# Kernel tuning notes

Measured on AMD Instinct MI355X. Metric: run time of the kernel, lower is better.

## Reference

```python
import jax, jax.numpy as jnp
import numpy as np

# Conv hyperparams (from init_kwargs)
STRIDE = (1, 1)
PADDING = (1, 1)
DILATION = (1, 1)

AQMIN, AQMAX = 0.0, 15.0   # uint4 activation range
WQMIN, WQMAX = -8.0, 7.0   # int4 weight range


def setup_inputs() -> dict:
    key = jax.random.key(0)
    k1, k2 = jax.random.split(key)
    # Activations in [0, 16) so uint4 quantization is non-trivial
    x = jax.random.uniform(k1, (32, 64, 112, 112), dtype=jnp.float32) * 16.0
    # Weights spread over int4 range
    w = jax.random.normal(k2, (128, 64, 3, 3), dtype=jnp.float32) * 4.0
    return {"x": x, "w": w}


def reference(x, w):
    # Quantize: activations -> uint4 [0,15], weights -> int4 [-8,7]
    q_in = jnp.clip(jnp.round(x), AQMIN, AQMAX)
    q_w = jnp.clip(jnp.round(w), WQMIN, WQMAX)
    # im2col unfold + matmul in the original == standard convolution.
    # Integer-valued fp32 math is exact here (|acc| << 2^24).
    out = jax.lax.conv_general_dilated(
        q_in, q_w,
        window_strides=STRIDE,
        padding=[(PADDING[0], PADDING[0]), (PADDING[1], PADDING[1])],
        rhs_dilation=DILATION,
        dimension_numbers=("NCHW", "OIHW", "NCHW"),
    )
    return out.astype(jnp.float32)  # [32, 128, 112, 112]
```

## Files before the change

kernel.cpp:

```cpp
#include <hip/hip_runtime.h>


#define CIN  64
#define HH   112
#define WW   112
#define HW   (HH * WW)
#define COUT 128
#define HP   114
#define WP   114
#define KTOT 576

#define XQ_BYTES (32 * HP * WP * 64)
#define NWBLK 288
#define NXBLK (32 * 57)
#define NCONV (32 * HH)

#define ROWB (WP * 64)
#define SLAB_BYTES (3 * ROWB)
#define SLAB_U16   (SLAB_BYTES / 16)

typedef __attribute__((ext_vector_type(4))) int int32x4;

__global__ __launch_bounds__(256) void k_prep(const float* __restrict__ x,
                                              const float* __restrict__ w,
                                              char* __restrict__ xq,
                                              char* __restrict__ wq) {
    const int bid = blockIdx.x, tid = threadIdx.x;
    if (bid < NWBLK) {
        int idx = bid * 256 + tid;
        int ks  = idx / 8192;
        int r2  = idx % 8192;
        int ct  = r2 / 1024;
        int r3  = r2 % 1024;
        int ln  = r3 / 16;
        int j   = r3 % 16;
        int o   = ct * 16 + (ln & 15);
        int c   = (ln >> 4) * 16 + j;
        int kh  = ks / 3, kw = ks % 3;
        float q = fminf(fmaxf(rintf(w[((o * CIN + c) * 3 + kh) * 3 + kw]), -8.0f), 7.0f);
        wq[idx] = (char)(int)q;
        return;
    }
    const int rid = bid - NWBLK;
    const int n  = rid / 57;
    const int hp = (rid % 57) * 2 + (tid >> 7);
    const int wp = tid & 127;
    if (wp >= WP) return;
    char* dst = xq + (((size_t)n * HP + hp) * WP + wp) * 64;
    int32x4* d4 = (int32x4*)dst;
    if (hp == 0 || hp == HP - 1 || wp == 0 || wp == WP - 1) {
#pragma unroll
        for (int i = 0; i < 4; ++i) d4[i] = (int32x4)(0);
        return;
    }
    const int h = hp - 1, ww = wp - 1;
    const float* px = x + (((size_t)n * CIN) * HH + h) * WW + ww;
    unsigned int buf[16];
#pragma unroll
    for (int cw = 0; cw < 16; ++cw) {
        unsigned int word = 0;
#pragma unroll
        for (int j = 0; j < 4; ++j) {
            float v = px[(size_t)(cw * 4 + j) * HW];
            float q = fminf(fmaxf(rintf(v), 0.0f), 15.0f);
            word |= ((unsigned int)(int)q) << (8 * j);
        }
        buf[cw] = word;
    }
#pragma unroll
    for (int i = 0; i < 4; ++i) {
        int32x4 v;
        v.x = (int)buf[i * 4 + 0];
        v.y = (int)buf[i * 4 + 1];
        v.z = (int)buf[i * 4 + 2];
        v.w = (int)buf[i * 4 + 3];
        d4[i] = v;
    }
}

__global__ __launch_bounds__(256, 4) void k_conv(const char* __restrict__ xq,
                                                 const char* __restrict__ wq,
                                                 float* __restrict__ out) {
    __shared__ char slab[SLAB_BYTES];

    const int tid = threadIdx.x;
    const int nid = (blockIdx.x & 7) * (NCONV / 8) + (blockIdx.x >> 3);
    const int n   = nid / HH;
    const int h   = nid % HH;

    const char* src = xq + (size_t)n * (HP * ROWB) + (size_t)h * ROWB;
#pragma unroll
    for (int k = 0; k < 6; ++k) {
        const int u = tid + k * 256;
        if (u < SLAB_U16)
            *(int32x4*)(&slab[u * 16]) = *(const int32x4*)(src + u * 16);
    }
    __syncthreads();

    const int wave = tid >> 6;
    const int lane = tid & 63;
    const int l15  = lane & 15;
    const int lk   = lane >> 4;
    const int Q    = wave;

    const char* wbase = wq + (Q * 2) * 1024 + lane * 16;

    int32x4 acc[7][2];
#pragma unroll
    for (int i = 0; i < 7; ++i) {
        acc[i][0] = (int32x4)(0);
        acc[i][1] = (int32x4)(0);
    }

    int32x4 b0[2], b1[2], b2[2];
    b0[0] = *(const int32x4*)(wbase);
    b0[1] = *(const int32x4*)(wbase + 1024);
    b1[0] = *(const int32x4*)(wbase + 8192);
    b1[1] = *(const int32x4*)(wbase + 8192 + 1024);

#pragma unroll
    for (int ks = 0; ks < 9; ++ks) {
        {
            const int ksn = (ks + 2 <= 8) ? ks + 2 : 8;
            b2[0] = *(const int32x4*)(wbase + ksn * 8192);
            b2[1] = *(const int32x4*)(wbase + ksn * 8192 + 1024);
        }
        const int kh = ks / 3, kw = ks % 3;
        const char* arow = &slab[((kh * WP) + l15 + kw) * 64 + lk * 16];
        int32x4 af[7];
#pragma unroll
        for (int wt = 0; wt < 7; ++wt)
            af[wt] = *(const int32x4*)(arow + wt * 1024);
#pragma unroll
        for (int tO = 0; tO < 2; ++tO)
#pragma unroll
            for (int wt = 0; wt < 7; ++wt)
                acc[wt][tO] = __builtin_amdgcn_mfma_i32_16x16x64_i8(af[wt], b0[tO], acc[wt][tO], 0, 0, 0);
        b0[0] = b1[0]; b0[1] = b1[1];
        b1[0] = b2[0]; b1[1] = b2[1];
    }

#pragma unroll
    for (int wt = 0; wt < 7; ++wt) {
#pragma unroll
        for (int tO = 0; tO < 2; ++tO) {
            const int co = Q * 32 + tO * 16 + l15;
            float4 v;
            v.x = (float)acc[wt][tO][0];
            v.y = (float)acc[wt][tO][1];
            v.z = (float)acc[wt][tO][2];
            v.w = (float)acc[wt][tO][3];
            *(float4*)(&out[(((size_t)n * COUT + co) * HH + h) * WW + wt * 16 + lk * 4]) = v;
        }
    }
}

extern "C" void kernel_launch(void* const* d_in, const int* in_sizes, int n_in,
                              void* d_out, int out_size, void* d_ws, size_t ws_size,
                              hipStream_t stream) {
    const float* x = (const float*)d_in[0];
    const float* w = (const float*)d_in[1];
    float* out = (float*)d_out;

    char* xq = (char*)d_ws;
    char* wq = xq + XQ_BYTES;

    hipLaunchKernelGGL(k_prep, dim3(NWBLK + NXBLK), dim3(256), 0, stream, x, w, xq, wq);
    hipLaunchKernelGGL(k_conv, dim3(NCONV), dim3(256), 0, stream, xq, wq, out);
}
```

Before: 92.14 us.

## Preload all conv weights into registers and stream output tiles per width chunk

The conv kernel now loads all nine kernel-position weight fragments into registers before the LDS slab load, so weight global loads overlap with the slab fill. The loop order changes from kernel position outer to width tile outer: each width tile loads its nine activation fragments, runs 18 MFMAs into two accumulators, and stores its output right away. This cuts the live accumulator count from 14 vectors to 2 and interleaves stores with compute. In exchange, weight register use grows and the MFMA dependency chains per accumulator become longer. Launch bounds drop from 4 to 3 blocks per CU.

Result: faster. 87.02 us, median of 2 (-5.6%).

```diff
diff --git a/kernel.cpp b/kernel.cpp
--- a/kernel.cpp
+++ b/kernel.cpp
@@ -78,7 +78,7 @@
     }
 }
 
-__global__ __launch_bounds__(256, 4) void k_conv(const char* __restrict__ xq,
+__global__ __launch_bounds__(256, 3) void k_conv(const char* __restrict__ xq,
                                                  const char* __restrict__ wq,
                                                  float* __restrict__ out) {
     __shared__ char slab[SLAB_BYTES];
@@ -87,6 +87,20 @@
     const int nid = (blockIdx.x & 7) * (NCONV / 8) + (blockIdx.x >> 3);
     const int n   = nid / HH;
     const int h   = nid % HH;
+
+    const int wave = tid >> 6;
+    const int lane = tid & 63;
+    const int l15  = lane & 15;
+    const int lk   = lane >> 4;
+    const int Q    = wave;
+
+    const char* wbase = wq + (Q * 2) * 1024 + lane * 16;
+    int32x4 wreg[9][2];
+#pragma unroll
+    for (int ks = 0; ks < 9; ++ks) {
+        wreg[ks][0] = *(const int32x4*)(wbase + ks * 8192);
+        wreg[ks][1] = *(const int32x4*)(wbase + ks * 8192 + 1024);
+    }
 
     const char* src = xq + (size_t)n * (HP * ROWB) + (size_t)h * ROWB;
 #pragma unroll
@@ -97,61 +111,28 @@
     }
     __syncthreads();
 
-    const int wave = tid >> 6;
-    const int lane = tid & 63;
-    const int l15  = lane & 15;
-    const int lk   = lane >> 4;
-    const int Q    = wave;
-
-    const char* wbase = wq + (Q * 2) * 1024 + lane * 16;
-
-    int32x4 acc[7][2];
-#pragma unroll
-    for (int i = 0; i < 7; ++i) {
-        acc[i][0] = (int32x4)(0);
-        acc[i][1] = (int32x4)(0);
-    }
-
-    int32x4 b0[2], b1[2], b2[2];
-    b0[0] = *(const int32x4*)(wbase);
-    b0[1] = *(const int32x4*)(wbase + 1024);
-    b1[0] = *(const int32x4*)(wbase + 8192);
-    b1[1] = *(const int32x4*)(wbase + 8192 + 1024);
-
-#pragma unroll
-    for (int ks = 0; ks < 9; ++ks) {
-        {
-            const int ksn = (ks + 2 <= 8) ? ks + 2 : 8;
-            b2[0] = *(const int32x4*)(wbase + ksn * 8192);
-            b2[1] = *(const int32x4*)(wbase + ksn * 8192 + 1024);
-        }
-        const int kh = ks / 3, kw = ks % 3;
-        const char* arow = &slab[((kh * WP) + l15 + kw) * 64 + lk * 16];
-        int32x4 af[7];
-#pragma unroll
-        for (int wt = 0; wt < 7; ++wt)
-            af[wt] = *(const int32x4*)(arow + wt * 1024);
-#pragma unroll
-        for (int tO = 0; tO < 2; ++tO)
-#pragma unroll
-            for (int wt = 0; wt < 7; ++wt)
-                acc[wt][tO] = __builtin_amdgcn_mfma_i32_16x16x64_i8(af[wt], b0[tO], acc[wt][tO], 0, 0, 0);
-        b0[0] = b1[0]; b0[1] = b1[1];
-        b1[0] = b2[0]; b1[1] = b2[1];
-    }
+    float* obase = out + (((size_t)n * COUT + Q * 32 + l15) * HH + h) * WW + lk * 4;
 
 #pragma unroll
     for (int wt = 0; wt < 7; ++wt) {
+        int32x4 af[9];
 #pragma unroll
-        for (int tO = 0; tO < 2; ++tO) {
-            const int co = Q * 32 + tO * 16 + l15;
-            float4 v;
-            v.x = (float)acc[wt][tO][0];
-            v.y = (float)acc[wt][tO][1];
-            v.z = (float)acc[wt][tO][2];
-            v.w = (float)acc[wt][tO][3];
-            *(float4*)(&out[(((size_t)n * COUT + co) * HH + h) * WW + wt * 16 + lk * 4]) = v;
+        for (int ks = 0; ks < 9; ++ks) {
+            const int kh = ks / 3, kw = ks % 3;
+            af[ks] = *(const int32x4*)(&slab[((kh * WP) + wt * 16 + l15 + kw) * 64 + lk * 16]);
         }
+        int32x4 a0 = (int32x4)(0);
+        int32x4 a1 = (int32x4)(0);
+#pragma unroll
+        for (int ks = 0; ks < 9; ++ks) {
+            a0 = __builtin_amdgcn_mfma_i32_16x16x64_i8(af[ks], wreg[ks][0], a0, 0, 0, 0);
+            a1 = __builtin_amdgcn_mfma_i32_16x16x64_i8(af[ks], wreg[ks][1], a1, 0, 0, 0);
+        }
+        float4 v0, v1;
+        v0.x = (float)a0[0]; v0.y = (float)a0[1]; v0.z = (float)a0[2]; v0.w = (float)a0[3];
+        v1.x = (float)a1[0]; v1.y = (float)a1[1]; v1.z = (float)a1[2]; v1.w = (float)a1[3];
+        *(float4*)(obase + wt * 16)            = v0;
+        *(float4*)(obase + 16 * HW + wt * 16)  = v1;
     }
 }
 
```

## Fuse activation quantization and conv into persistent kernel with per-image flags

Applied to the files above, without the earlier changes.

Moves activation quantization out of the prep kernel into a persistent main kernel (768 blocks) that first processes quantize items and then conv items. Each conv item spins on a per-image atomic counter until all 57 row-pair blocks of that image are written, so conv work for early images can overlap quantization of later ones. This removes the kernel boundary between the quantize and conv stages. In exchange it adds spin-waiting, acquire/release fences, and a residency assumption: the persistent grid must be co-resident or the spin-waits could deadlock.

New measurement: 334.9 us. +263.4%, slower.

```diff
diff --git a/kernel.cpp b/kernel.cpp
--- a/kernel.cpp
+++ b/kernel.cpp
@@ -11,9 +11,13 @@
 #define KTOT 576
 
 #define XQ_BYTES (32 * HP * WP * 64)
+#define WQ_BYTES (COUT * KTOT)
 #define NWBLK 288
-#define NXBLK (32 * 57)
-#define NCONV (32 * HH)
+
+#define NACT   (32 * 57)
+#define NCONVI (32 * HH)
+#define NITEMS (NACT + NCONVI)
+#define GPERS  768
 
 #define ROWB (WP * 64)
 #define SLAB_BYTES (3 * ROWB)
@@ -21,10 +25,9 @@
 
 typedef __attribute__((ext_vector_type(4))) int int32x4;
 
-__global__ __launch_bounds__(256) void k_prep(const float* __restrict__ x,
-                                              const float* __restrict__ w,
-                                              char* __restrict__ xq,
-                                              char* __restrict__ wq) {
+__global__ __launch_bounds__(256) void k_init(const float* __restrict__ w,
+                                              char* __restrict__ wq,
+                                              int* __restrict__ flags) {
     const int bid = blockIdx.x, tid = threadIdx.x;
     if (bid < NWBLK) {
         int idx = bid * 256 + tid;
@@ -41,116 +44,136 @@
         wq[idx] = (char)(int)q;
         return;
     }
-    const int rid = bid - NWBLK;
-    const int n  = rid / 57;
-    const int hp = (rid % 57) * 2 + (tid >> 7);
-    const int wp = tid & 127;
-    if (wp >= WP) return;
-    char* dst = xq + (((size_t)n * HP + hp) * WP + wp) * 64;
-    int32x4* d4 = (int32x4*)dst;
-    if (hp == 0 || hp == HP - 1 || wp == 0 || wp == WP - 1) {
-#pragma unroll
-        for (int i = 0; i < 4; ++i) d4[i] = (int32x4)(0);
-        return;
-    }
-    const int h = hp - 1, ww = wp - 1;
-    const float* px = x + (((size_t)n * CIN) * HH + h) * WW + ww;
-    unsigned int buf[16];
-#pragma unroll
-    for (int cw = 0; cw < 16; ++cw) {
-        unsigned int word = 0;
-#pragma unroll
-        for (int j = 0; j < 4; ++j) {
-            float v = px[(size_t)(cw * 4 + j) * HW];
-            float q = fminf(fmaxf(rintf(v), 0.0f), 15.0f);
-            word |= ((unsigned int)(int)q) << (8 * j);
-        }
-        buf[cw] = word;
-    }
-#pragma unroll
-    for (int i = 0; i < 4; ++i) {
-        int32x4 v;
-        v.x = (int)buf[i * 4 + 0];
-        v.y = (int)buf[i * 4 + 1];
-        v.z = (int)buf[i * 4 + 2];
-        v.w = (int)buf[i * 4 + 3];
-        d4[i] = v;
-    }
+    if (tid < 64) flags[tid] = 0;
 }
 
-__global__ __launch_bounds__(256, 4) void k_conv(const char* __restrict__ xq,
+__global__ __launch_bounds__(256, 4) void k_main(const float* __restrict__ x,
+                                                 char* __restrict__ xq,
                                                  const char* __restrict__ wq,
-                                                 float* __restrict__ out) {
+                                                 float* __restrict__ out,
+                                                 int* __restrict__ flags) {
     __shared__ char slab[SLAB_BYTES];
+    const int tid = threadIdx.x;
 
-    const int tid = threadIdx.x;
-    const int nid = (blockIdx.x & 7) * (NCONV / 8) + (blockIdx.x >> 3);
-    const int n   = nid / HH;
-    const int h   = nid % HH;
+    for (int item = blockIdx.x; item < NITEMS; item += GPERS) {
+        if (item < NACT) {
+            const int n  = item / 57;
+            const int pr = item % 57;
+            const int hp = pr * 2 + (tid >> 7);
+            const int wp = tid & 127;
+            if (wp < WP) {
+                char* dst = xq + (((size_t)n * HP + hp) * WP + wp) * 64;
+                int32x4* d4 = (int32x4*)dst;
+                if (hp == 0 || hp == HP - 1 || wp == 0 || wp == WP - 1) {
+#pragma unroll
+                    for (int i = 0; i < 4; ++i) d4[i] = (int32x4)(0);
+                } else {
+                    const int h = hp - 1, ww = wp - 1;
+                    const float* px = x + (((size_t)n * CIN) * HH + h) * WW + ww;
+                    unsigned int buf[16];
+#pragma unroll
+                    for (int cw = 0; cw < 16; ++cw) {
+                        unsigned int word = 0;
+#pragma unroll
+                        for (int j = 0; j < 4; ++j) {
+                            float v = px[(size_t)(cw * 4 + j) * HW];
+                            float q = fminf(fmaxf(rintf(v), 0.0f), 15.0f);
+                            word |= ((unsigned int)(int)q) << (8 * j);
+                        }
+                        buf[cw] = word;
+                    }
+#pragma unroll
+                    for (int i = 0; i < 4; ++i) {
+                        int32x4 v;
+                        v.x = (int)buf[i * 4 + 0];
+                        v.y = (int)buf[i * 4 + 1];
+                        v.z = (int)buf[i * 4 + 2];
+                        v.w = (int)buf[i * 4 + 3];
+                        d4[i] = v;
+                    }
+                }
+            }
+            __syncthreads();
+            if (tid == 0)
+                __hip_atomic_fetch_add(&flags[n], 1, __ATOMIC_RELEASE,
+                                       __HIP_MEMORY_SCOPE_AGENT);
+        } else {
+            const int nid = item - NACT;
+            const int n   = nid / HH;
+            const int h   = nid % HH;
 
-    const char* src = xq + (size_t)n * (HP * ROWB) + (size_t)h * ROWB;
+            if (tid == 0) {
+                while (__hip_atomic_load(&flags[n], __ATOMIC_RELAXED,
+                                         __HIP_MEMORY_SCOPE_AGENT) < 57)
+                    __builtin_amdgcn_s_sleep(2);
+            }
+            __syncthreads();
+            __builtin_amdgcn_fence(__ATOMIC_ACQUIRE, "agent");
+
+            const char* src = xq + (size_t)n * (HP * ROWB) + (size_t)h * ROWB;
 #pragma unroll
-    for (int k = 0; k < 6; ++k) {
-        const int u = tid + k * 256;
-        if (u < SLAB_U16)
-            *(int32x4*)(&slab[u * 16]) = *(const int32x4*)(src + u * 16);
-    }
-    __syncthreads();
+            for (int k = 0; k < 6; ++k) {
+                const int u = tid + k * 256;
+                if (u < SLAB_U16)
+                    *(int32x4*)(&slab[u * 16]) = *(const int32x4*)(src + u * 16);
+            }
+            __syncthreads();
 
-    const int wave = tid >> 6;
-    const int lane = tid & 63;
-    const int l15  = lane & 15;
-    const int lk   = lane >> 4;
-    const int Q    = wave;
+            const int wave = tid >> 6;
+            const int lane = tid & 63;
+            const int l15  = lane & 15;
+            const int lk   = lane >> 4;
+            const int Q    = wave;
 
-    const char* wbase = wq + (Q * 2) * 1024 + lane * 16;
+            const char* wbase = wq + (Q * 2) * 1024 + lane * 16;
 
-    int32x4 acc[7][2];
+            int32x4 acc[7][2];
 #pragma unroll
-    for (int i = 0; i < 7; ++i) {
-        acc[i][0] = (int32x4)(0);
-        acc[i][1] = (int32x4)(0);
-    }
+            for (int i = 0; i < 7; ++i) {
+                acc[i][0] = (int32x4)(0);
+                acc[i][1] = (int32x4)(0);
+            }
 
-    int32x4 b0[2], b1[2], b2[2];
-    b0[0] = *(const int32x4*)(wbase);
-    b0[1] = *(const int32x4*)(wbase + 1024);
-    b1[0] = *(const int32x4*)(wbase + 8192);
-    b1[1] = *(const int32x4*)(wbase + 8192 + 1024);
+            int32x4 b0[2], b1[2], b2[2];
+            b0[0] = *(const int32x4*)(wbase);
+            b0[1] = *(const int32x4*)(wbase + 1024);
+            b1[0] = *(const int32x4*)(wbase + 8192);
+            b1[1] = *(const int32x4*)(wbase + 8192 + 1024);
 
 #pragma unroll
-    for (int ks = 0; ks < 9; ++ks) {
-        {
-            const int ksn = (ks + 2 <= 8) ? ks + 2 : 8;
-            b2[0] = *(const int32x4*)(wbase + ksn * 8192);
-            b2[1] = *(const int32x4*)(wbase + ksn * 8192 + 1024);
-        }
-        const int kh = ks / 3, kw = ks % 3;
-        const char* arow = &slab[((kh * WP) + l15 + kw) * 64 + lk * 16];
-        int32x4 af[7];
+            for (int ks = 0; ks < 9; ++ks) {
+                const int ksn = (ks + 2 <= 8) ? ks + 2 : 8;
+                b2[0] = *(const int32x4*)(wbase + ksn * 8192);
+                b2[1] = *(const int32x4*)(wbase + ksn * 8192 + 1024);
+                const int kh = ks / 3, kw = ks % 3;
+                const char* arow = &slab[((kh * WP) + l15 + kw) * 64 + lk * 16];
+                int32x4 af[7];
 #pragma unroll
-        for (int wt = 0; wt < 7; ++wt)
-            af[wt] = *(const int32x4*)(arow + wt * 1024);
+                for (int wt = 0; wt < 7; ++wt)
+                    af[wt] = *(const int32x4*)(arow + wt * 1024);
 #pragma unroll
-        for (int tO = 0; tO < 2; ++tO)
+                for (int tO = 0; tO < 2; ++tO)
 #pragma unroll
-            for (int wt = 0; wt < 7; ++wt)
-                acc[wt][tO] = __builtin_amdgcn_mfma_i32_16x16x64_i8(af[wt], b0[tO], acc[wt][tO], 0, 0, 0);
-        b0[0] = b1[0]; b0[1] = b1[1];
-        b1[0] = b2[0]; b1[1] = b2[1];
-    }
+                    for (int wt = 0; wt < 7; ++wt)
+                        acc[wt][tO] = __builtin_amdgcn_mfma_i32_16x16x64_i8(af[wt], b0[tO], acc[wt][tO], 0, 0, 0);
+                b0[0] = b1[0]; b0[1] = b1[1];
+                b1[0] = b2[0]; b1[1] = b2[1];
+            }
 
 #pragma unroll
-    for (int wt = 0; wt < 7; ++wt) {
+            for (int wt = 0; wt < 7; ++wt) {
 #pragma unroll
-        for (int tO = 0; tO < 2; ++tO) {
-            const int co = Q * 32 + tO * 16 + l15;
-            float4 v;
-            v.x = (float)acc[wt][tO][0];
-            v.y = (float)acc[wt][tO][1];
-            v.z = (float)acc[wt][tO][2];
-            v.w = (float)acc[wt][tO][3];
-            *(float4*)(&out[(((size_t)n * COUT + co) * HH + h) * WW + wt * 16 + lk * 4]) = v;
+                for (int tO = 0; tO < 2; ++tO) {
+                    const int co = Q * 32 + tO * 16 + l15;
+                    float4 v;
+                    v.x = (float)acc[wt][tO][0];
+                    v.y = (float)acc[wt][tO][1];
+                    v.z = (float)acc[wt][tO][2];
+                    v.w = (float)acc[wt][tO][3];
+                    *(float4*)(&out[(((size_t)n * COUT + co) * HH + h) * WW + wt * 16 + lk * 4]) = v;
+                }
+            }
+            __syncthreads();
         }
     }
 }
@@ -164,7 +187,8 @@
 
     char* xq = (char*)d_ws;
     char* wq = xq + XQ_BYTES;
+    int* flags = (int*)(wq + WQ_BYTES);
 
-    hipLaunchKernelGGL(k_prep, dim3(NWBLK + NXBLK), dim3(256), 0, stream, x, w, xq, wq);
-    hipLaunchKernelGGL(k_conv, dim3(NCONV), dim3(256), 0, stream, xq, wq, out);
+    hipLaunchKernelGGL(k_init, dim3(NWBLK + 1), dim3(256), 0, stream, w, wq, flags);
+    hipLaunchKernelGGL(k_main, dim3(GPERS), dim3(256), 0, stream, x, xq, wq, out, flags);
 }
```
